# Performance work log

Measured on AMD Instinct MI355X. Metric: run time of the kernel, lower is better.

## Reference

```python
import jax, jax.numpy as jnp
import numpy as np

B, Q, C, H, W = 2, 10, 64, 256, 256   # input is (B*Q, C, H, W); N ico nodes = Q*H*W
K = 9                                  # KNN kernel size
L_H, L_W = 180, 360                    # ERP grid (180/delta x 360/delta), delta=1
L = L_H * L_W
N = Q * H * W


def setup_inputs() -> dict:
    key = jax.random.key(0)
    k1, k2, k3, k4, k5, k6 = jax.random.split(key, 6)
    x = jax.random.normal(k1, (B * Q, C, H, W), dtype=jnp.float32)
    idx = jax.random.randint(k2, (L, K), 0, N, dtype=jnp.int64)  # zero-based seqnumkmin
    att_w = jax.random.normal(k3, (K, 2, K), dtype=jnp.float32) * 0.1  # Conv2d(2,K,(1,K)) weight
    att_b = jax.random.normal(k4, (K,), dtype=jnp.float32) * 0.1
    tc_w = jax.random.normal(k5, (C, K), dtype=jnp.float32) * 0.1     # depthwise Conv2d(C,C,(1,K),groups=C)
    tc_b = jax.random.normal(k6, (C,), dtype=jnp.float32) * 0.1
    return {"x": x, "idx": idx, "att_w": att_w, "att_b": att_b, "tc_w": tc_w, "tc_b": tc_b}


def reference(x, idx, att_w, att_b, tc_w, tc_b):
    # (b q) c h w -> b c (q h w)
    b = x.shape[0] // Q
    xf = x.reshape(b, Q, C, H, W).transpose(0, 2, 1, 3, 4).reshape(b, C, N)
    # KNN gather: (b, C, L, K)
    xe = xf[:, :, idx]
    # spatial attention: mean/max over channels -> (b, 2, L, K)
    stats = jnp.stack([xe.mean(axis=1), xe.max(axis=1)], axis=1)
    # conv (1,K) over neighbor axis: out (b, K, L)
    att = jax.nn.sigmoid(jnp.einsum('bilk,cik->bcl', stats, att_w) + att_b[None, :, None])
    att = att.transpose(0, 2, 1)[:, None, :, :]  # b 1 L K
    xe = att * xe + xe
    # depthwise grouped conv over neighbor axis -> (b, C, L)
    out = jnp.einsum('bclk,ck->bcl', xe, tc_w) + tc_b[None, :, None]
    return out.reshape(b, C, L_H, L_W)
```

## Files before the change

### kernel.cpp

```cpp
#include <hip/hip_runtime.h>
#include <hip/hip_bf16.h>
#include <math.h>

#define QQ   10
#define CC   64
#define HWSZ 65536
#define NPOS 655360
#define LL   64800
#define KK   9

__global__ __launch_bounds__(256) void k_transpose_stats(
    const float* __restrict__ x, __hip_bfloat16* __restrict__ xt,
    float2* __restrict__ stats) {
  __shared__ float tile[64][65];
  __shared__ float sred[4][64];
  __shared__ float mred[4][64];
  const int t    = threadIdx.x;
  const int lane = t & 63;
  const int wid  = t >> 6;
  const int hw_base = blockIdx.x * 64;
  const int bq = blockIdx.y;
  const float* xp = x + (size_t)bq * CC * HWSZ + hw_base;

#pragma unroll
  for (int i = 0; i < 4; ++i) {
    int linear = t + i * 256;
    int row  = linear >> 4;
    int col4 = (linear & 15) << 2;
    const float4 v = *(const float4*)(xp + (size_t)row * HWSZ + col4);
    tile[row][col4 + 0] = v.x;
    tile[row][col4 + 1] = v.y;
    tile[row][col4 + 2] = v.z;
    tile[row][col4 + 3] = v.w;
  }
  __syncthreads();

  const int b = bq / QQ, q = bq % QQ;
  const size_t n_base = (size_t)q * HWSZ + hw_base;
  __hip_bfloat16* xtb = xt + (size_t)b * NPOS * CC;

  const int c0  = (lane & 15) << 2;
  const int sub = lane >> 4;
#pragma unroll
  for (int j = 0; j < 4; ++j) {
    const int p = wid * 16 + j * 4 + sub;
    const float v0 = tile[c0 + 0][p];
    const float v1 = tile[c0 + 1][p];
    const float v2 = tile[c0 + 2][p];
    const float v3 = tile[c0 + 3][p];
    union { __hip_bfloat162 h; unsigned u; } lo, hi;
    lo.h = __float22bfloat162_rn(make_float2(v0, v1));
    hi.h = __float22bfloat162_rn(make_float2(v2, v3));
    uint2 pk; pk.x = lo.u; pk.y = hi.u;
    *(uint2*)(xtb + (n_base + p) * CC + c0) = pk;
  }

  {
    const int pos = lane;
    const int cc0 = wid * 16;
    float psum = tile[cc0][pos];
    float pmax = psum;
#pragma unroll
    for (int c = 1; c < 16; ++c) {
      const float v = tile[cc0 + c][pos];
      psum += v;
      pmax = fmaxf(pmax, v);
    }
    sred[wid][pos] = psum;
    mred[wid][pos] = pmax;
  }
  __syncthreads();
  if (wid == 0) {
    const int pos = lane;
    float2 sm;
    sm.x = sred[0][pos] + sred[1][pos] + sred[2][pos] + sred[3][pos];
    sm.y = fmaxf(fmaxf(mred[0][pos], mred[1][pos]),
                 fmaxf(mred[2][pos], mred[3][pos]));
    stats[(size_t)b * NPOS + n_base + pos] = sm;
  }
}

__global__ __launch_bounds__(256) void k_att(
    const float2* __restrict__ stats, const int* __restrict__ idx,
    const float* __restrict__ att_w, const float* __restrict__ att_b,
    float* __restrict__ watt) {
  __shared__ float aw[2 * KK * KK + KK];
  const int t = threadIdx.x;
  if (t < 2 * KK * KK) aw[t] = att_w[t];
  else if (t < 2 * KK * KK + KK) aw[t] = att_b[t - 2 * KK * KK];
  __syncthreads();

  const int tg = blockIdx.x * 256 + t;
  if (tg >= 2 * LL) return;
  const int b = tg / LL;
  const int l = tg - b * LL;
  const float2* st = stats + (size_t)b * NPOS;

  float mean[KK], mx[KK];
#pragma unroll
  for (int k = 0; k < KK; ++k) {
    const int n = idx[l * KK + k];
    const float2 sm = st[n];
    mean[k] = sm.x * (1.0f / 64.0f);
    mx[k]   = sm.y;
  }

  float* wp = watt + (size_t)tg * KK;
#pragma unroll
  for (int h = 0; h < KK; ++h) {
    float logit = aw[2 * KK * KK + h];
#pragma unroll
    for (int k = 0; k < KK; ++k) {
      logit = fmaf(mean[k], aw[h * 2 * KK + k], logit);
      logit = fmaf(mx[k],   aw[h * 2 * KK + KK + k], logit);
    }
    wp[h] = 1.0f + 1.0f / (1.0f + __expf(-logit));
  }
}

__global__ __launch_bounds__(256) void k_gather_out(
    const __hip_bfloat16* __restrict__ xt, const int* __restrict__ idx,
    const float* __restrict__ watt, const float* __restrict__ tc_w,
    const float* __restrict__ tc_b, float* __restrict__ out) {
  const int blk    = blockIdx.x;
  const int b      = blk / (LL / 32);
  const int l_base = (blk % (LL / 32)) * 32;
  const int t = threadIdx.x, lane = t & 63, wid = t >> 6;
  const int half = lane >> 5, lh = lane & 31;
  __shared__ float res[64][33];

  float tw0[KK], tw1[KK];
#pragma unroll
  for (int k = 0; k < KK; ++k) {
    tw0[k] = tc_w[(2 * lh) * KK + k];
    tw1[k] = tc_w[(2 * lh + 1) * KK + k];
  }
  const float tb0 = tc_b[2 * lh];
  const float tb1 = tc_b[2 * lh + 1];

  const unsigned* xtb = (const unsigned*)(xt + (size_t)b * NPOS * CC);
  const float* wb = watt + (size_t)b * LL * KK;
  const int kl = lh < KK ? lh : KK - 1;

#pragma unroll
  for (int j = 0; j < 4; ++j) {
    const int myl = l_base + wid * 8 + j * 2 + half;
    const int   nk = idx[myl * KK + kl];
    const float wv = wb[myl * KK + kl];

    float a0 = 0.0f, a1 = 0.0f;
#pragma unroll
    for (int k = 0; k < KK; ++k) {
      const int   src = half * 32 + k;
      const int   n   = __shfl(nk, src);
      const float wk  = __shfl(wv, src);
      const unsigned u = xtb[(size_t)n * 32 + lh];
      const float f0 = __uint_as_float(u << 16);
      const float f1 = __uint_as_float(u & 0xffff0000u);
      a0 = fmaf(wk * tw0[k], f0, a0);
      a1 = fmaf(wk * tw1[k], f1, a1);
    }
    const int li = wid * 8 + j * 2 + half;
    res[2 * lh][li]     = a0 + tb0;
    res[2 * lh + 1][li] = a1 + tb1;
  }
  __syncthreads();

  const int c  = t >> 2;
  const int q4 = t & 3;
#pragma unroll
  for (int rep = 0; rep < 2; ++rep) {
    const int lo = rep * 16 + q4 * 4;
    float4 o;
    o.x = res[c][lo + 0];
    o.y = res[c][lo + 1];
    o.z = res[c][lo + 2];
    o.w = res[c][lo + 3];
    *(float4*)(out + ((size_t)b * CC + c) * LL + l_base + lo) = o;
  }
}

extern "C" void kernel_launch(void* const* d_in, const int* in_sizes, int n_in,
                              void* d_out, int out_size, void* d_ws, size_t ws_size,
                              hipStream_t stream) {
  const float* x     = (const float*)d_in[0];
  const int*   idx   = (const int*)d_in[1];
  const float* att_w = (const float*)d_in[2];
  const float* att_b = (const float*)d_in[3];
  const float* tc_w  = (const float*)d_in[4];
  const float* tc_b  = (const float*)d_in[5];
  float* out = (float*)d_out;

  __hip_bfloat16* xt = (__hip_bfloat16*)d_ws;
  float2* stats = (float2*)(xt + (size_t)2 * NPOS * CC);
  float* watt = (float*)(stats + (size_t)2 * NPOS);

  dim3 g1(HWSZ / 64, 2 * QQ);
  k_transpose_stats<<<g1, 256, 0, stream>>>(x, xt, stats);

  dim3 g2((2 * LL + 255) / 256);
  k_att<<<g2, 256, 0, stream>>>(stats, idx, att_w, att_b, watt);

  dim3 g3(2 * (LL / 32));
  k_gather_out<<<g3, 256, 0, stream>>>(xt, idx, watt, tc_w, tc_b, out);
}
```

Before: 548.5 us.

## Mask unreferenced nodes in transpose and fuse attention into gather kernel

Builds a byte mask of the ico nodes referenced by idx, so the transpose/stats kernel writes bf16 rows and stats only for nodes that are actually gathered. This cuts the write traffic of the transposed copy: about 583k lookups into 655k nodes leaves a sizeable fraction untouched. The separate attention kernel is removed. Its logits and sigmoid are now computed per block in shared memory inside the gather kernel, which drops the watt buffer round trip and one launch. In exchange it adds two small mask kernels and extra syncs and shared-memory staging in the gather kernel.

```diff
diff --git a/kernel.cpp b/kernel.cpp
--- a/kernel.cpp
+++ b/kernel.cpp
@@ -9,9 +9,19 @@
 #define LL   64800
 #define KK   9
 
+__global__ __launch_bounds__(256) void k_mask_zero(uint4* __restrict__ m) {
+  m[blockIdx.x * 256 + threadIdx.x] = make_uint4(0u, 0u, 0u, 0u);
+}
+
+__global__ __launch_bounds__(256) void k_mask_set(
+    const int* __restrict__ idx, unsigned char* __restrict__ m) {
+  const int i = blockIdx.x * 256 + threadIdx.x;
+  if (i < LL * KK) m[idx[i]] = 1;
+}
+
 __global__ __launch_bounds__(256) void k_transpose_stats(
-    const float* __restrict__ x, __hip_bfloat16* __restrict__ xt,
-    float2* __restrict__ stats) {
+    const float* __restrict__ x, const unsigned char* __restrict__ mask,
+    __hip_bfloat16* __restrict__ xt, float2* __restrict__ stats) {
   __shared__ float tile[64][65];
   __shared__ float sred[4][64];
   __shared__ float mred[4][64];
@@ -44,15 +54,17 @@
 #pragma unroll
   for (int j = 0; j < 4; ++j) {
     const int p = wid * 16 + j * 4 + sub;
-    const float v0 = tile[c0 + 0][p];
-    const float v1 = tile[c0 + 1][p];
-    const float v2 = tile[c0 + 2][p];
-    const float v3 = tile[c0 + 3][p];
-    union { __hip_bfloat162 h; unsigned u; } lo, hi;
-    lo.h = __float22bfloat162_rn(make_float2(v0, v1));
-    hi.h = __float22bfloat162_rn(make_float2(v2, v3));
-    uint2 pk; pk.x = lo.u; pk.y = hi.u;
-    *(uint2*)(xtb + (n_base + p) * CC + c0) = pk;
+    if (mask[n_base + p]) {
+      const float v0 = tile[c0 + 0][p];
+      const float v1 = tile[c0 + 1][p];
+      const float v2 = tile[c0 + 2][p];
+      const float v3 = tile[c0 + 3][p];
+      union { __hip_bfloat162 h; unsigned u; } lo, hi;
+      lo.h = __float22bfloat162_rn(make_float2(v0, v1));
+      hi.h = __float22bfloat162_rn(make_float2(v2, v3));
+      uint2 pk; pk.x = lo.u; pk.y = hi.u;
+      *(uint2*)(xtb + (n_base + p) * CC + c0) = pk;
+    }
   }
 
   {
@@ -72,62 +84,55 @@
   __syncthreads();
   if (wid == 0) {
     const int pos = lane;
-    float2 sm;
-    sm.x = sred[0][pos] + sred[1][pos] + sred[2][pos] + sred[3][pos];
-    sm.y = fmaxf(fmaxf(mred[0][pos], mred[1][pos]),
-                 fmaxf(mred[2][pos], mred[3][pos]));
-    stats[(size_t)b * NPOS + n_base + pos] = sm;
-  }
-}
-
-__global__ __launch_bounds__(256) void k_att(
-    const float2* __restrict__ stats, const int* __restrict__ idx,
-    const float* __restrict__ att_w, const float* __restrict__ att_b,
-    float* __restrict__ watt) {
-  __shared__ float aw[2 * KK * KK + KK];
-  const int t = threadIdx.x;
-  if (t < 2 * KK * KK) aw[t] = att_w[t];
-  else if (t < 2 * KK * KK + KK) aw[t] = att_b[t - 2 * KK * KK];
-  __syncthreads();
-
-  const int tg = blockIdx.x * 256 + t;
-  if (tg >= 2 * LL) return;
-  const int b = tg / LL;
-  const int l = tg - b * LL;
-  const float2* st = stats + (size_t)b * NPOS;
-
-  float mean[KK], mx[KK];
-#pragma unroll
-  for (int k = 0; k < KK; ++k) {
-    const int n = idx[l * KK + k];
-    const float2 sm = st[n];
-    mean[k] = sm.x * (1.0f / 64.0f);
-    mx[k]   = sm.y;
-  }
-
-  float* wp = watt + (size_t)tg * KK;
-#pragma unroll
-  for (int h = 0; h < KK; ++h) {
-    float logit = aw[2 * KK * KK + h];
-#pragma unroll
-    for (int k = 0; k < KK; ++k) {
-      logit = fmaf(mean[k], aw[h * 2 * KK + k], logit);
-      logit = fmaf(mx[k],   aw[h * 2 * KK + KK + k], logit);
-    }
-    wp[h] = 1.0f + 1.0f / (1.0f + __expf(-logit));
+    if (mask[n_base + pos]) {
+      float2 sm;
+      sm.x = sred[0][pos] + sred[1][pos] + sred[2][pos] + sred[3][pos];
+      sm.y = fmaxf(fmaxf(mred[0][pos], mred[1][pos]),
+                   fmaxf(mred[2][pos], mred[3][pos]));
+      stats[(size_t)b * NPOS + n_base + pos] = sm;
+    }
   }
 }
 
 __global__ __launch_bounds__(256) void k_gather_out(
-    const __hip_bfloat16* __restrict__ xt, const int* __restrict__ idx,
-    const float* __restrict__ watt, const float* __restrict__ tc_w,
+    const __hip_bfloat16* __restrict__ xt, const float2* __restrict__ stats,
+    const int* __restrict__ idx, const float* __restrict__ att_w,
+    const float* __restrict__ att_b, const float* __restrict__ tc_w,
     const float* __restrict__ tc_b, float* __restrict__ out) {
   const int blk    = blockIdx.x;
   const int b      = blk / (LL / 32);
   const int l_base = (blk % (LL / 32)) * 32;
   const int t = threadIdx.x, lane = t & 63, wid = t >> 6;
   const int half = lane >> 5, lh = lane & 31;
-  __shared__ float res[64][33];
+  __shared__ float  res[64][33];
+  __shared__ float2 nw[32][KK];
+  __shared__ float  sms[32][KK], smm[32][KK];
+  __shared__ float  aw[2 * KK * KK + KK];
+
+  if (t < 2 * KK * KK + KK)
+    aw[t] = (t < 2 * KK * KK) ? att_w[t] : att_b[t - 2 * KK * KK];
+
+  const float2* stb = stats + (size_t)b * NPOS;
+  for (int i = t; i < 32 * KK; i += 256) {
+    const int ll = i / KK, k = i - ll * KK;
+    const int n = idx[(l_base + ll) * KK + k];
+    nw[ll][k].x = __int_as_float(n);
+    const float2 sm = stb[n];
+    sms[ll][k] = sm.x;
+    smm[ll][k] = sm.y;
+  }
+  __syncthreads();
+
+  for (int i = t; i < 32 * KK; i += 256) {
+    const int ll = i / KK, h = i - ll * KK;
+    float logit = aw[2 * KK * KK + h];
+#pragma unroll
+    for (int k = 0; k < KK; ++k) {
+      logit = fmaf(sms[ll][k] * (1.0f / 64.0f), aw[h * 2 * KK + k], logit);
+      logit = fmaf(smm[ll][k], aw[h * 2 * KK + KK + k], logit);
+    }
+    nw[ll][h].y = 1.0f + 1.0f / (1.0f + __expf(-logit));
+  }
 
   float tw0[KK], tw1[KK];
 #pragma unroll
@@ -137,32 +142,24 @@
   }
   const float tb0 = tc_b[2 * lh];
   const float tb1 = tc_b[2 * lh + 1];
-
-  const unsigned* xtb = (const unsigned*)(xt + (size_t)b * NPOS * CC);
-  const float* wb = watt + (size_t)b * LL * KK;
-  const int kl = lh < KK ? lh : KK - 1;
-
+  __syncthreads();
+
+  const unsigned* xtb = (const unsigned*)xt + (size_t)b * NPOS * 32;
 #pragma unroll
   for (int j = 0; j < 4; ++j) {
-    const int myl = l_base + wid * 8 + j * 2 + half;
-    const int   nk = idx[myl * KK + kl];
-    const float wv = wb[myl * KK + kl];
-
+    const int ll = wid * 8 + j * 2 + half;
     float a0 = 0.0f, a1 = 0.0f;
 #pragma unroll
     for (int k = 0; k < KK; ++k) {
-      const int   src = half * 32 + k;
-      const int   n   = __shfl(nk, src);
-      const float wk  = __shfl(wv, src);
+      const float2 p = nw[ll][k];
+      const int   n  = __float_as_int(p.x);
+      const float wk = p.y;
       const unsigned u = xtb[(size_t)n * 32 + lh];
-      const float f0 = __uint_as_float(u << 16);
-      const float f1 = __uint_as_float(u & 0xffff0000u);
-      a0 = fmaf(wk * tw0[k], f0, a0);
-      a1 = fmaf(wk * tw1[k], f1, a1);
-    }
-    const int li = wid * 8 + j * 2 + half;
-    res[2 * lh][li]     = a0 + tb0;
-    res[2 * lh + 1][li] = a1 + tb1;
+      a0 = fmaf(wk * tw0[k], __uint_as_float(u << 16), a0);
+      a1 = fmaf(wk * tw1[k], __uint_as_float(u & 0xffff0000u), a1);
+    }
+    res[2 * lh][ll]     = a0 + tb0;
+    res[2 * lh + 1][ll] = a1 + tb1;
   }
   __syncthreads();
 
@@ -193,14 +190,15 @@
 
   __hip_bfloat16* xt = (__hip_bfloat16*)d_ws;
   float2* stats = (float2*)(xt + (size_t)2 * NPOS * CC);
-  float* watt = (float*)(stats + (size_t)2 * NPOS);
+  unsigned char* mask = (unsigned char*)(stats + (size_t)2 * NPOS);
+
+  k_mask_zero<<<NPOS / (16 * 256), 256, 0, stream>>>((uint4*)mask);
+  k_mask_set<<<(LL * KK + 255) / 256, 256, 0, stream>>>(idx, mask);
 
   dim3 g1(HWSZ / 64, 2 * QQ);
-  k_transpose_stats<<<g1, 256, 0, stream>>>(x, xt, stats);
-
-  dim3 g2((2 * LL + 255) / 256);
-  k_att<<<g2, 256, 0, stream>>>(stats, idx, att_w, att_b, watt);
-
-  dim3 g3(2 * (LL / 32));
-  k_gather_out<<<g3, 256, 0, stream>>>(xt, idx, watt, tc_w, tc_b, out);
-}
+  k_transpose_stats<<<g1, 256, 0, stream>>>(x, mask, xt, stats);
+
+  dim3 g2(2 * (LL / 32));
+  k_gather_out<<<g2, 256, 0, stream>>>(xt, stats, idx, att_w, att_b,
+                                       tc_w, tc_b, out);
+}
```

New measurement: 519.2 us. -5.4%, faster.
